# Kernel tuning notes

Hardware: AMD Instinct MI355X
Metric: run time of the kernel (lower is better)

## Reference

```python
import jax, jax.numpy as jnp
import numpy as np

B, T, I, H, C = 8192, 784, 1, 30, 10


def setup_inputs() -> dict:
    key = jax.random.key(0)
    ks = jax.random.split(key, 7)
    s_ih = 1.0 / np.sqrt(H)
    return {
        "x": jax.random.normal(ks[0], (B, T, I), dtype=jnp.float32),
        "W_ih": jax.random.uniform(ks[1], (H, I), jnp.float32, -s_ih, s_ih),
        "W_hh": jax.random.uniform(ks[2], (H, H), jnp.float32, -s_ih, s_ih),
        "b_ih": jax.random.uniform(ks[3], (H,), jnp.float32, -s_ih, s_ih),
        "b_hh": jax.random.uniform(ks[4], (H,), jnp.float32, -s_ih, s_ih),
        "W_fc": jax.random.uniform(ks[5], (C, H), jnp.float32, -s_ih, s_ih),
        "b_fc": jax.random.uniform(ks[6], (C,), jnp.float32, -s_ih, s_ih),
    }


def reference(x, W_ih, W_hh, b_ih, b_hh, W_fc, b_fc):
    # x: [B, T, I] -> scan over time. h_t = tanh(x_t W_ih^T + b_ih + h W_hh^T + b_hh)
    xs = jnp.swapaxes(x, 0, 1)  # [T, B, I]
    h0 = jnp.zeros((x.shape[0], W_hh.shape[0]), dtype=x.dtype)
    bias = b_ih + b_hh  # [H]

    def step(h, xt):
        h_new = jnp.tanh(xt @ W_ih.T + h @ W_hh.T + bias)
        return h_new, None

    hT, _ = jax.lax.scan(step, h0, xs)  # hT: [B, H] == out[:, -1, :]
    return hT @ W_fc.T + b_fc  # [B, C]
```

## Files before the change

### kernel.cpp

```cpp
#include <hip/hip_runtime.h>


#define BB 8192
#define TT 784
#define HH 30
#define HP 32
#define CC 10
#define TPB 16
#define ROWS 2
#define NB 16
#define LSTR 36

__global__ __launch_bounds__(256, 2)
void rnn_scan_kernel(const float* __restrict__ x,
                     const float* __restrict__ W_ih,
                     const float* __restrict__ W_hh,
                     const float* __restrict__ b_ih,
                     const float* __restrict__ b_hh,
                     const float* __restrict__ W_fc,
                     const float* __restrict__ b_fc,
                     float* __restrict__ out) {
    __shared__ float hbuf[NB * LSTR];

    const int tid = threadIdx.x;
    const int bl  = tid >> 4;
    const int r   = tid & 15;
    const int i0  = r * ROWS;
    const int b   = blockIdx.x * NB + bl;

    float w[ROWS][HP];
    float bias[ROWS], wih[ROWS];
#pragma unroll
    for (int rr = 0; rr < ROWS; ++rr) {
        const int i = i0 + rr;
        const bool valid = (i < HH);
#pragma unroll
        for (int j = 0; j < HP; ++j)
            w[rr][j] = (valid && (j < HH)) ? W_hh[i * HH + j] : 0.0f;
        bias[rr] = valid ? (b_ih[i] + b_hh[i]) : 0.0f;
        wih[rr]  = valid ? W_ih[i] : 0.0f;
    }

    float* hp = &hbuf[bl * LSTR];
    *(float2*)&hp[i0] = make_float2(0.f, 0.f);
    __builtin_amdgcn_wave_barrier();

    const float* xb = x + (size_t)b * TT;
    float4 xq = *(const float4*)(xb);

    for (int q = 0; q < TT / 4; ++q) {
        float4 nxt = (q + 1 < TT / 4) ? *(const float4*)(xb + (q + 1) * 4)
                                      : make_float4(0.f, 0.f, 0.f, 0.f);
#pragma unroll
        for (int u = 0; u < 4; ++u) {
            const float xt = (u == 0) ? xq.x : (u == 1) ? xq.y
                           : (u == 2) ? xq.z : xq.w;
            float a0 = bias[0] + xt * wih[0], a0b = 0.f;
            float a1 = bias[1] + xt * wih[1], a1b = 0.f;
#pragma unroll
            for (int jq = 0; jq < HP / 4; ++jq) {
                const float4 hq = *(const float4*)(hp + jq * 4);
                a0  += w[0][jq * 4 + 0] * hq.x;
                a0b += w[0][jq * 4 + 1] * hq.y;
                a0  += w[0][jq * 4 + 2] * hq.z;
                a0b += w[0][jq * 4 + 3] * hq.w;
                a1  += w[1][jq * 4 + 0] * hq.x;
                a1b += w[1][jq * 4 + 1] * hq.y;
                a1  += w[1][jq * 4 + 2] * hq.z;
                a1b += w[1][jq * 4 + 3] * hq.w;
            }
            const float acc0 = a0 + a0b;
            const float acc1 = a1 + a1b;
            float2 hn;
            hn.x = 1.0f - 2.0f * __builtin_amdgcn_rcpf(__expf(2.0f * acc0) + 1.0f);
            hn.y = 1.0f - 2.0f * __builtin_amdgcn_rcpf(__expf(2.0f * acc1) + 1.0f);
            __builtin_amdgcn_wave_barrier();
            *(float2*)&hp[i0] = hn;
            __builtin_amdgcn_wave_barrier();
        }
        xq = nxt;
    }

    if (r < CC) {
        const int c = r;
        float acc = b_fc[c];
#pragma unroll
        for (int j = 0; j < HH; ++j)
            acc += W_fc[c * HH + j] * hp[j];
        out[(size_t)b * CC + c] = acc;
    }
}

extern "C" void kernel_launch(void* const* d_in, const int* in_sizes, int n_in,
                              void* d_out, int out_size, void* d_ws, size_t ws_size,
                              hipStream_t stream) {
    const float* x    = (const float*)d_in[0];
    const float* W_ih = (const float*)d_in[1];
    const float* W_hh = (const float*)d_in[2];
    const float* b_ih = (const float*)d_in[3];
    const float* b_hh = (const float*)d_in[4];
    const float* W_fc = (const float*)d_in[5];
    const float* b_fc = (const float*)d_in[6];

    hipLaunchKernelGGL(rnn_scan_kernel,
                       dim3(BB / NB), dim3(NB * TPB), 0, stream,
                       x, W_ih, W_hh, b_ih, b_hh, W_fc, b_fc,
                       (float*)d_out);
}
```

Before: 291.6 us.

## Broadcast hidden state with DPP row_bcast instead of LDS round-trips

Hidden state now stays in registers, and each timestep broadcasts lane k's pair of h values to the other lanes of its 16-lane row with DPP row_newbcast. This replaces the per-step LDS store, wave barriers and float4 LDS reads. The matvec is also restructured into packed two-wide FMAs (f32x2) with split accumulators, so the compiler can emit v_pk_fma_f32. The cost is 32 DPP moves per step, each carrying its own data-hazard latency, and the code depends on the DPP row broadcast control being valid on this architecture.

Measured after the change: 423.9 us. +45.4%, slower.

```diff
diff --git a/kernel.cpp b/kernel.cpp
--- a/kernel.cpp
+++ b/kernel.cpp
@@ -4,12 +4,21 @@
 #define BB 8192
 #define TT 784
 #define HH 30
-#define HP 32
 #define CC 10
-#define TPB 16
-#define ROWS 2
 #define NB 16
 #define LSTR 36
+
+typedef __attribute__((ext_vector_type(2))) float f32x2;
+
+#define BC(v, k) __uint_as_float((unsigned)__builtin_amdgcn_update_dpp( \
+        0, (int)__float_as_uint(v), 0x150 | (k), 0xF, 0xF, false))
+
+#define KSTEP(k, P0, P1) {            \
+        f32x2 hh;                     \
+        hh.x = BC(h0, k);             \
+        hh.y = BC(h1, k);             \
+        P0 += w0[k] * hh;             \
+        P1 += w1[k] * hh; }
 
 __global__ __launch_bounds__(256, 2)
 void rnn_scan_kernel(const float* __restrict__ x,
@@ -25,25 +34,25 @@
     const int tid = threadIdx.x;
     const int bl  = tid >> 4;
     const int r   = tid & 15;
-    const int i0  = r * ROWS;
+    const int i0  = r * 2;
     const int b   = blockIdx.x * NB + bl;
 
-    float w[ROWS][HP];
-    float bias[ROWS], wih[ROWS];
+    f32x2 w0[16], w1[16];
+    const bool v0 = (i0 < HH), v1 = (i0 + 1 < HH);
 #pragma unroll
-    for (int rr = 0; rr < ROWS; ++rr) {
-        const int i = i0 + rr;
-        const bool valid = (i < HH);
-#pragma unroll
-        for (int j = 0; j < HP; ++j)
-            w[rr][j] = (valid && (j < HH)) ? W_hh[i * HH + j] : 0.0f;
-        bias[rr] = valid ? (b_ih[i] + b_hh[i]) : 0.0f;
-        wih[rr]  = valid ? W_ih[i] : 0.0f;
+    for (int k = 0; k < 16; ++k) {
+        const int c0 = 2 * k, c1 = 2 * k + 1;
+        w0[k].x = (v0 && c0 < HH) ? W_hh[i0 * HH + c0] : 0.0f;
+        w0[k].y = (v0 && c1 < HH) ? W_hh[i0 * HH + c1] : 0.0f;
+        w1[k].x = (v1 && c0 < HH) ? W_hh[(i0 + 1) * HH + c0] : 0.0f;
+        w1[k].y = (v1 && c1 < HH) ? W_hh[(i0 + 1) * HH + c1] : 0.0f;
     }
+    const float bias0 = v0 ? (b_ih[i0] + b_hh[i0]) : 0.0f;
+    const float bias1 = v1 ? (b_ih[i0 + 1] + b_hh[i0 + 1]) : 0.0f;
+    const float wih0  = v0 ? W_ih[i0] : 0.0f;
+    const float wih1  = v1 ? W_ih[i0 + 1] : 0.0f;
 
-    float* hp = &hbuf[bl * LSTR];
-    *(float2*)&hp[i0] = make_float2(0.f, 0.f);
-    __builtin_amdgcn_wave_barrier();
+    float h0 = 0.0f, h1 = 0.0f;
 
     const float* xb = x + (size_t)b * TT;
     float4 xq = *(const float4*)(xb);
@@ -55,31 +64,31 @@
         for (int u = 0; u < 4; ++u) {
             const float xt = (u == 0) ? xq.x : (u == 1) ? xq.y
                            : (u == 2) ? xq.z : xq.w;
-            float a0 = bias[0] + xt * wih[0], a0b = 0.f;
-            float a1 = bias[1] + xt * wih[1], a1b = 0.f;
-#pragma unroll
-            for (int jq = 0; jq < HP / 4; ++jq) {
-                const float4 hq = *(const float4*)(hp + jq * 4);
-                a0  += w[0][jq * 4 + 0] * hq.x;
-                a0b += w[0][jq * 4 + 1] * hq.y;
-                a0  += w[0][jq * 4 + 2] * hq.z;
-                a0b += w[0][jq * 4 + 3] * hq.w;
-                a1  += w[1][jq * 4 + 0] * hq.x;
-                a1b += w[1][jq * 4 + 1] * hq.y;
-                a1  += w[1][jq * 4 + 2] * hq.z;
-                a1b += w[1][jq * 4 + 3] * hq.w;
-            }
-            const float acc0 = a0 + a0b;
-            const float acc1 = a1 + a1b;
-            float2 hn;
-            hn.x = 1.0f - 2.0f * __builtin_amdgcn_rcpf(__expf(2.0f * acc0) + 1.0f);
-            hn.y = 1.0f - 2.0f * __builtin_amdgcn_rcpf(__expf(2.0f * acc1) + 1.0f);
-            __builtin_amdgcn_wave_barrier();
-            *(float2*)&hp[i0] = hn;
-            __builtin_amdgcn_wave_barrier();
+            const float base0 = bias0 + xt * wih0;
+            const float base1 = bias1 + xt * wih1;
+            f32x2 p0a = {0.f, 0.f}, p0b = {0.f, 0.f};
+            f32x2 p1a = {0.f, 0.f}, p1b = {0.f, 0.f};
+            KSTEP( 0, p0a, p1a) KSTEP( 1, p0b, p1b)
+            KSTEP( 2, p0a, p1a) KSTEP( 3, p0b, p1b)
+            KSTEP( 4, p0a, p1a) KSTEP( 5, p0b, p1b)
+            KSTEP( 6, p0a, p1a) KSTEP( 7, p0b, p1b)
+            KSTEP( 8, p0a, p1a) KSTEP( 9, p0b, p1b)
+            KSTEP(10, p0a, p1a) KSTEP(11, p0b, p1b)
+            KSTEP(12, p0a, p1a) KSTEP(13, p0b, p1b)
+            KSTEP(14, p0a, p1a) KSTEP(15, p0b, p1b)
+            const f32x2 s0 = p0a + p0b;
+            const f32x2 s1 = p1a + p1b;
+            const float acc0 = base0 + s0.x + s0.y;
+            const float acc1 = base1 + s1.x + s1.y;
+            h0 = 1.0f - 2.0f * __builtin_amdgcn_rcpf(__expf(2.0f * acc0) + 1.0f);
+            h1 = 1.0f - 2.0f * __builtin_amdgcn_rcpf(__expf(2.0f * acc1) + 1.0f);
         }
         xq = nxt;
     }
+
+    float* hp = &hbuf[bl * LSTR];
+    *(float2*)&hp[i0] = make_float2(h0, h1);
+    __builtin_amdgcn_wave_barrier();
 
     if (r < CC) {
         const int c = r;
@@ -103,7 +112,7 @@
     const float* b_fc = (const float*)d_in[6];
 
     hipLaunchKernelGGL(rnn_scan_kernel,
-                       dim3(BB / NB), dim3(NB * TPB), 0, stream,
+                       dim3(BB / NB), dim3(NB * 16), 0, stream,
                        x, W_ih, W_hh, b_ih, b_hh, W_fc, b_fc,
                        (float*)d_out);
 }
```

## Compute recurrent matvec with split-bf16 MFMA, keeping hidden state in registers

Applied to the files above, without the earlier changes.

Replaces the per-thread FP32 dot products over an LDS-held hidden state with 16x16x32 bf16 MFMA instructions. Weights and hidden state are split into high and low bf16 parts, and three MFMA products approximate FP32 accuracy. The permuted row layout makes each MFMA output land where the next step's B operand needs it, so the hidden state stays in registers and the LDS round-trip and wave barriers go away. The cost is bf16x3 error (the low x low term is dropped) and one 64-thread wave per block with waves_per_eu set to 1, which may lower latency hiding across the long sequential chain.

After: 289.1 us. Within noise of the previous version (-0.9%).

```diff
diff --git a/kernel.cpp b/kernel.cpp
--- a/kernel.cpp
+++ b/kernel.cpp
@@ -4,14 +4,27 @@
 #define BB 8192
 #define TT 784
 #define HH 30
-#define HP 32
 #define CC 10
-#define TPB 16
-#define ROWS 2
-#define NB 16
-#define LSTR 36
 
-__global__ __launch_bounds__(256, 2)
+typedef __attribute__((ext_vector_type(8))) short  bf16x8;
+typedef __attribute__((ext_vector_type(4))) float  f32x4;
+typedef __attribute__((ext_vector_type(4))) unsigned uint4v;
+
+__device__ __forceinline__ float tanh_fast(float a) {
+    return 1.0f - 2.0f * __builtin_amdgcn_rcpf(__expf(2.0f * a) + 1.0f);
+}
+
+#define BPAIR(p0, p1, hp, lp) do {                                          \
+    asm("v_cvt_pk_bf16_f32 %0, %1, %2" : "=v"(hp) : "v"(p0), "v"(p1));      \
+    const float _h0 = __uint_as_float((hp) << 16);                          \
+    const float _h1 = __uint_as_float((hp) & 0xffff0000u);                  \
+    const float _l0 = (p0) - _h0;                                           \
+    const float _l1 = (p1) - _h1;                                           \
+    asm("v_cvt_pk_bf16_f32 %0, %1, %2" : "=v"(lp) : "v"(_l0), "v"(_l1));    \
+} while (0)
+
+__global__ __launch_bounds__(64)
+__attribute__((amdgpu_waves_per_eu(1, 1)))
 void rnn_scan_kernel(const float* __restrict__ x,
                      const float* __restrict__ W_ih,
                      const float* __restrict__ W_hh,
@@ -20,74 +33,100 @@
                      const float* __restrict__ W_fc,
                      const float* __restrict__ b_fc,
                      float* __restrict__ out) {
-    __shared__ float hbuf[NB * LSTR];
+    const int lane = threadIdx.x & 63;
+    const int n    = lane & 15;
+    const int g    = lane >> 4;
+    const int b    = blockIdx.x * 16 + n;
 
-    const int tid = threadIdx.x;
-    const int bl  = tid >> 4;
-    const int r   = tid & 15;
-    const int i0  = r * ROWS;
-    const int b   = blockIdx.x * NB + bl;
+    const int r1 = 8 * (n >> 2) + (n & 3);
+    const int r2 = r1 + 4;
+    unsigned a1h[4], a1l[4], a2h[4], a2l[4];
+#pragma unroll
+    for (int d = 0; d < 4; ++d) {
+        const int k0 = 8 * g + 2 * d, k1 = k0 + 1;
+        const float w1a = (k0 < HH) ? W_hh[r1 * HH + k0] : 0.f;
+        const float w1b = (k1 < HH) ? W_hh[r1 * HH + k1] : 0.f;
+        const float w2a = (r2 < HH && k0 < HH) ? W_hh[r2 * HH + k0] : 0.f;
+        const float w2b = (r2 < HH && k1 < HH) ? W_hh[r2 * HH + k1] : 0.f;
+        const unsigned u1a = __float_as_uint(w1a), u1b = __float_as_uint(w1b);
+        const unsigned u2a = __float_as_uint(w2a), u2b = __float_as_uint(w2b);
+        a1h[d] = (u1b & 0xffff0000u) | (u1a >> 16);
+        a2h[d] = (u2b & 0xffff0000u) | (u2a >> 16);
+        const float l1a = w1a - __uint_as_float(u1a & 0xffff0000u);
+        const float l1b = w1b - __uint_as_float(u1b & 0xffff0000u);
+        const float l2a = w2a - __uint_as_float(u2a & 0xffff0000u);
+        const float l2b = w2b - __uint_as_float(u2b & 0xffff0000u);
+        a1l[d] = (__float_as_uint(l1b) & 0xffff0000u) | (__float_as_uint(l1a) >> 16);
+        a2l[d] = (__float_as_uint(l2b) & 0xffff0000u) | (__float_as_uint(l2a) >> 16);
+    }
+    bf16x8 A1h = __builtin_bit_cast(bf16x8, (uint4v){a1h[0], a1h[1], a1h[2], a1h[3]});
+    bf16x8 A1l = __builtin_bit_cast(bf16x8, (uint4v){a1l[0], a1l[1], a1l[2], a1l[3]});
+    bf16x8 A2h = __builtin_bit_cast(bf16x8, (uint4v){a2h[0], a2h[1], a2h[2], a2h[3]});
+    bf16x8 A2l = __builtin_bit_cast(bf16x8, (uint4v){a2l[0], a2l[1], a2l[2], a2l[3]});
+    asm volatile("" : "+v"(A1h), "+v"(A1l), "+v"(A2h), "+v"(A2l));
 
-    float w[ROWS][HP];
-    float bias[ROWS], wih[ROWS];
+    float bias1[4], wih1[4], bias2[4], wih2[4];
 #pragma unroll
-    for (int rr = 0; rr < ROWS; ++rr) {
-        const int i = i0 + rr;
-        const bool valid = (i < HH);
-#pragma unroll
-        for (int j = 0; j < HP; ++j)
-            w[rr][j] = (valid && (j < HH)) ? W_hh[i * HH + j] : 0.0f;
-        bias[rr] = valid ? (b_ih[i] + b_hh[i]) : 0.0f;
-        wih[rr]  = valid ? W_ih[i] : 0.0f;
+    for (int r = 0; r < 4; ++r) {
+        const int q1 = 8 * g + r;
+        bias1[r] = b_ih[q1] + b_hh[q1];
+        wih1[r]  = W_ih[q1];
+        const int q2 = q1 + 4;
+        bias2[r] = (q2 < HH) ? (b_ih[q2] + b_hh[q2]) : 0.f;
+        wih2[r]  = (q2 < HH) ? W_ih[q2] : 0.f;
+        asm volatile("" : "+v"(bias1[r]), "+v"(wih1[r]), "+v"(bias2[r]), "+v"(wih2[r]));
     }
 
-    float* hp = &hbuf[bl * LSTR];
-    *(float2*)&hp[i0] = make_float2(0.f, 0.f);
-    __builtin_amdgcn_wave_barrier();
+    float h0 = 0.f, h1 = 0.f, h2 = 0.f, h3 = 0.f;
+    float h4 = 0.f, h5 = 0.f, h6 = 0.f, h7 = 0.f;
 
-    const float* xb = x + (size_t)b * TT;
-    float4 xq = *(const float4*)(xb);
+    const float* xp = x + (size_t)b * TT;
+    float4 xq = *(const float4*)xp;
 
-    for (int q = 0; q < TT / 4; ++q) {
-        float4 nxt = (q + 1 < TT / 4) ? *(const float4*)(xb + (q + 1) * 4)
-                                      : make_float4(0.f, 0.f, 0.f, 0.f);
+    for (int qq = 0; qq < TT / 4; ++qq) {
+        const float4 nxt = (qq + 1 < TT / 4) ? *(const float4*)(xp + (qq + 1) * 4)
+                                             : make_float4(0.f, 0.f, 0.f, 0.f);
 #pragma unroll
         for (int u = 0; u < 4; ++u) {
             const float xt = (u == 0) ? xq.x : (u == 1) ? xq.y
                            : (u == 2) ? xq.z : xq.w;
-            float a0 = bias[0] + xt * wih[0], a0b = 0.f;
-            float a1 = bias[1] + xt * wih[1], a1b = 0.f;
-#pragma unroll
-            for (int jq = 0; jq < HP / 4; ++jq) {
-                const float4 hq = *(const float4*)(hp + jq * 4);
-                a0  += w[0][jq * 4 + 0] * hq.x;
-                a0b += w[0][jq * 4 + 1] * hq.y;
-                a0  += w[0][jq * 4 + 2] * hq.z;
-                a0b += w[0][jq * 4 + 3] * hq.w;
-                a1  += w[1][jq * 4 + 0] * hq.x;
-                a1b += w[1][jq * 4 + 1] * hq.y;
-                a1  += w[1][jq * 4 + 2] * hq.z;
-                a1b += w[1][jq * 4 + 3] * hq.w;
-            }
-            const float acc0 = a0 + a0b;
-            const float acc1 = a1 + a1b;
-            float2 hn;
-            hn.x = 1.0f - 2.0f * __builtin_amdgcn_rcpf(__expf(2.0f * acc0) + 1.0f);
-            hn.y = 1.0f - 2.0f * __builtin_amdgcn_rcpf(__expf(2.0f * acc1) + 1.0f);
-            __builtin_amdgcn_wave_barrier();
-            *(float2*)&hp[i0] = hn;
-            __builtin_amdgcn_wave_barrier();
+            f32x4 acc1 = { fmaf(xt, wih1[0], bias1[0]), fmaf(xt, wih1[1], bias1[1]),
+                           fmaf(xt, wih1[2], bias1[2]), fmaf(xt, wih1[3], bias1[3]) };
+            f32x4 acc2 = { fmaf(xt, wih2[0], bias2[0]), fmaf(xt, wih2[1], bias2[1]),
+                           fmaf(xt, wih2[2], bias2[2]), fmaf(xt, wih2[3], bias2[3]) };
+            unsigned bh0, bh1, bh2, bh3, bl0, bl1, bl2, bl3;
+            BPAIR(h0, h1, bh0, bl0);
+            BPAIR(h2, h3, bh1, bl1);
+            BPAIR(h4, h5, bh2, bl2);
+            BPAIR(h6, h7, bh3, bl3);
+            const bf16x8 Bh = __builtin_bit_cast(bf16x8, (uint4v){bh0, bh1, bh2, bh3});
+            const bf16x8 Bl = __builtin_bit_cast(bf16x8, (uint4v){bl0, bl1, bl2, bl3});
+            acc1 = __builtin_amdgcn_mfma_f32_16x16x32_bf16(A1h, Bh, acc1, 0, 0, 0);
+            acc2 = __builtin_amdgcn_mfma_f32_16x16x32_bf16(A2h, Bh, acc2, 0, 0, 0);
+            acc1 = __builtin_amdgcn_mfma_f32_16x16x32_bf16(A1h, Bl, acc1, 0, 0, 0);
+            acc2 = __builtin_amdgcn_mfma_f32_16x16x32_bf16(A2h, Bl, acc2, 0, 0, 0);
+            acc1 = __builtin_amdgcn_mfma_f32_16x16x32_bf16(A1l, Bh, acc1, 0, 0, 0);
+            acc2 = __builtin_amdgcn_mfma_f32_16x16x32_bf16(A2l, Bh, acc2, 0, 0, 0);
+            h0 = tanh_fast(acc1[0]); h1 = tanh_fast(acc1[1]);
+            h2 = tanh_fast(acc1[2]); h3 = tanh_fast(acc1[3]);
+            h4 = tanh_fast(acc2[0]); h5 = tanh_fast(acc2[1]);
+            h6 = tanh_fast(acc2[2]); h7 = tanh_fast(acc2[3]);
         }
         xq = nxt;
     }
 
-    if (r < CC) {
-        const int c = r;
-        float acc = b_fc[c];
+    const float hreg[8] = {h0, h1, h2, h3, h4, h5, h6, h7};
 #pragma unroll
-        for (int j = 0; j < HH; ++j)
-            acc += W_fc[c * HH + j] * hp[j];
-        out[(size_t)b * CC + c] = acc;
+    for (int c = 0; c < CC; ++c) {
+        float p = 0.f;
+#pragma unroll
+        for (int j = 0; j < 8; ++j) {
+            const int k = 8 * g + j;
+            if (k < HH) p = fmaf(W_fc[c * HH + k], hreg[j], p);
+        }
+        p += __shfl_xor(p, 16);
+        p += __shfl_xor(p, 32);
+        if (g == 0) out[(size_t)b * CC + c] = p + b_fc[c];
     }
 }
 
@@ -103,7 +142,7 @@
     const float* b_fc = (const float*)d_in[6];
 
     hipLaunchKernelGGL(rnn_scan_kernel,
-                       dim3(BB / NB), dim3(NB * TPB), 0, stream,
+                       dim3(BB / 16), dim3(64), 0, stream,
                        x, W_ih, W_hh, b_ih, b_hh, W_fc, b_fc,
                        (float*)d_out);
 }
```
